# Kernel optimization log

Hardware: AMD Instinct MI355X
Metric: run time of the kernel (lower is better)

Reference implementation:

```python
import jax, jax.numpy as jnp
import numpy as np

DIM = 2048
HEAD_DIM = 128
NHEADS = DIM // HEAD_DIM
ROTARY_BASE = 10000.0
EPS = 1e-6


def rmsnorm(x):
    return x * jax.lax.rsqrt(jnp.mean(x * x, axis=-1, keepdims=True) + EPS)


def make_freqs():
    # (1/base)**linspace(0,1,head_dim//4) concatenated with head_dim//4 zeros
    f = (1.0 / ROTARY_BASE) ** jnp.linspace(0.0, 1.0, HEAD_DIM // 4, dtype=jnp.float32)
    return jnp.concatenate([f, jnp.zeros(HEAD_DIM // 4, dtype=jnp.float32)])  # [head_dim//2]


def rotary(x_NTHD, shift=0):
    T = x_NTHD.shape[1]
    freqs = make_freqs()
    theta = jnp.arange(shift, shift + T, dtype=jnp.float32)[:, None] * freqs[None, :]  # [T, d]
    cos = jnp.cos(theta)[None, :, None, :]
    sin = jnp.sin(theta)[None, :, None, :]
    x1, x2 = jnp.split(x_NTHD, 2, axis=-1)
    y1 = x1 * cos + x2 * sin
    y2 = -x1 * sin + x2 * cos
    return jnp.concatenate([y1, y2], axis=-1)


def setup_inputs() -> dict:
    key = jax.random.key(0)
    ks = jax.random.split(key, 7)
    N, T = 4, 2048
    sd = 1.0 / np.sqrt(DIM)
    x = jax.random.normal(ks[0], (N, T, DIM), dtype=jnp.float32)
    qkv_w = jnp.fmod(jax.random.normal(ks[1], (3, DIM, DIM), dtype=jnp.float32), 2.0) * (sd / 2)
    o_w = jax.random.normal(ks[2], (DIM, DIM), dtype=jnp.float32) * sd
    o_scale = jax.random.normal(ks[3], (DIM,), dtype=jnp.float32) * 0.02
    mlp_w1 = jax.random.normal(ks[4], (4 * DIM, DIM), dtype=jnp.float32) * sd
    mlp_w2 = jax.random.normal(ks[5], (DIM, 4 * DIM), dtype=jnp.float32) * (1.0 / np.sqrt(4 * DIM))
    mlp_scale = jax.random.normal(ks[6], (DIM,), dtype=jnp.float32) * 0.02
    return {"x": x, "qkv_w": qkv_w, "o_w": o_w, "o_scale": o_scale,
            "mlp_w1": mlp_w1, "mlp_w2": mlp_w2, "mlp_scale": mlp_scale}


def reference(x, qkv_w, o_w, o_scale, mlp_w1, mlp_w2, mlp_scale):
    N, T, _ = x.shape
    residual = x
    # RMSNorm -> fused QKV projection
    qkv = rmsnorm(x) @ qkv_w.reshape(3 * DIM, DIM).T            # [N,T,3*dim]
    qkv = qkv.reshape(N, T, 3 * NHEADS, HEAD_DIM)
    q, k, v = jnp.split(qkv, 3, axis=-2)                        # each [N,T,H,hd]
    q, k = rmsnorm(q), rmsnorm(k)                               # QK-norm over head_dim
    q, k = rotary(q), rotary(k)                                 # shift=0 (no kv cache)
    # causal SDPA
    scale = 1.0 / np.sqrt(HEAD_DIM)
    scores = jnp.einsum("bqhd,bkhd->bhqk", q, k) * scale
    mask = jnp.tril(jnp.ones((T, T), dtype=bool))
    scores = jnp.where(mask[None, None], scores, -jnp.inf)
    attn = jax.nn.softmax(scores, axis=-1)
    o = jnp.einsum("bhqk,bkhd->bqhd", attn, v).reshape(N, T, DIM)
    x = residual + (o @ o_w.T) * o_scale
    # MLP: RMSNorm -> up -> relu^2 -> down (scaled)
    h = rmsnorm(x) @ mlp_w1.T
    h = jnp.square(jax.nn.relu(h))
    x = x + (h @ mlp_w2.T) * mlp_scale
    return x, k, v
```

## Files before the change

kernel.cpp:

```cpp
#include <hip/hip_runtime.h>
#include <hip/hip_bf16.h>
#include <cstdint>
#include <cstddef>

typedef unsigned short ushort_t;
typedef __attribute__((ext_vector_type(8))) __bf16 bf16x8;
typedef __attribute__((ext_vector_type(4))) float f32x4;
typedef __attribute__((ext_vector_type(4))) unsigned int u32x4;
typedef __attribute__((ext_vector_type(2))) unsigned int u32x2;

#define LOG2E 1.44269504088896f

__device__ __forceinline__ float bf2f(unsigned short u) {
  union { unsigned int i; float f; } w; w.i = ((unsigned int)u) << 16; return w.f;
}
__device__ __forceinline__ unsigned short f2bf(float f) {
  union { float f; unsigned int i; } w; w.f = f;
  unsigned int u = w.i;
  u += 0x7fffu + ((u >> 16) & 1);
  return (unsigned short)(u >> 16);
}
__device__ __forceinline__ void gld_lds16(const void* g, void* l) {
  __builtin_amdgcn_global_load_lds(
      (const __attribute__((address_space(1))) unsigned int*)g,
      (__attribute__((address_space(3))) unsigned int*)l, 16, 0, 0);
}
__device__ __forceinline__ int swz(int row, int byteoff) {
  return byteoff ^ ((row & 7) << 4);
}

__global__ __launch_bounds__(256)
void cvt_bf16(const float* __restrict__ in, ushort_t* __restrict__ outp, int n) {
  const int i = (blockIdx.x * 256 + threadIdx.x) * 4;
  if (i >= n) return;
  const float4 d = *(const float4*)(in + i);
  u32x2 o;
  o[0] = (unsigned int)f2bf(d.x) | ((unsigned int)f2bf(d.y) << 16);
  o[1] = (unsigned int)f2bf(d.z) | ((unsigned int)f2bf(d.w) << 16);
  *(u32x2*)(outp + i) = o;
}

__device__ __forceinline__ void stage_half(const ushort_t* __restrict__ gsrc,
                                           size_t rstride, ushort_t* ldst, int tid) {
#pragma unroll
  for (int i = 0; i < 2; i++) {
    const int c = i * 512 + tid;
    const int r = c >> 3, col = c & 7;
    gld_lds16(gsrc + (size_t)r * rstride + ((col ^ (r & 7)) << 3), ldst + c * 8);
  }
}

template <int EPI, typename OutT>
__global__ __launch_bounds__(512, 2)
void gemm_bt256(const ushort_t* __restrict__ A, const ushort_t* __restrict__ B,
                OutT* __restrict__ C, const float* __restrict__ Res,
                const float* __restrict__ Scale, int M, int N, int K) {
  __shared__ ushort_t As[2][256 * 64];
  __shared__ ushort_t Bs[2][256 * 64];
  const int tid = threadIdx.x;
  const int wave = tid >> 6, lane = tid & 63;
  const int quad = lane >> 4, l16 = lane & 15;
  const int ntn = N >> 8;
  const int nwg = (M >> 8) * ntn;
  const int lin = blockIdx.y * gridDim.x + blockIdx.x;
  const int wid = (lin & 7) * (nwg >> 3) + (lin >> 3);
  const int bn = (wid % ntn) << 8;
  const int bm = (wid / ntn) << 8;
  const int wm = (wave >> 2) * 128, wn = (wave & 3) * 64;

  f32x4 acc[8][4] = {};

  const ushort_t* aB = A + (size_t)bm * K;
  const ushort_t* bB = B + (size_t)bn * K;
  const int nk = K >> 6;

  stage_half(aB, K, &As[0][0], tid);
  stage_half(aB + (size_t)128 * K, K, &As[0][8192], tid);
  stage_half(bB, K, &Bs[0][0], tid);
  stage_half(bB + (size_t)128 * K, K, &Bs[0][8192], tid);
  asm volatile("s_waitcnt vmcnt(0)" ::: "memory");
  __builtin_amdgcn_sched_barrier(0);
  __builtin_amdgcn_s_barrier();

  for (int t = 0; t < nk; ++t) {
    const int cur = t & 1, nb = cur ^ 1;
    const ushort_t* Ac = &As[cur][0];
    const ushort_t* Bc = &Bs[cur][0];
    const int k0n = (t + 1) << 6;
    const bool pf = (t + 1 < nk);
#pragma unroll
    for (int q = 0; q < 4; q++) {
      const int mh = q >> 1, nh = q & 1;
      bf16x8 af[4][2], bfq[2][2];
#pragma unroll
      for (int j = 0; j < 4; j++) {
        const int row = wm + (mh * 4 + j) * 16 + l16;
#pragma unroll
        for (int ks = 0; ks < 2; ks++)
          af[j][ks] = *(const bf16x8*)&Ac[row * 64 + (swz(row, ks * 64 + quad * 16) >> 1)];
      }
#pragma unroll
      for (int j = 0; j < 2; j++) {
        const int row = wn + (nh * 2 + j) * 16 + l16;
#pragma unroll
        for (int ks = 0; ks < 2; ks++)
          bfq[j][ks] = *(const bf16x8*)&Bc[row * 64 + (swz(row, ks * 64 + quad * 16) >> 1)];
      }
      if (pf) {
        if (q == 0)      stage_half(aB + k0n, K, &As[nb][0], tid);
        else if (q == 1) stage_half(aB + (size_t)128 * K + k0n, K, &As[nb][8192], tid);
        else if (q == 2) {
          stage_half(bB + k0n, K, &Bs[nb][0], tid);
          stage_half(bB + (size_t)128 * K + k0n, K, &Bs[nb][8192], tid);
        }
      }
      __builtin_amdgcn_sched_barrier(0);
      __builtin_amdgcn_s_barrier();
      __builtin_amdgcn_s_setprio(1);
#pragma unroll
      for (int j = 0; j < 4; j++)
#pragma unroll
        for (int n2 = 0; n2 < 2; n2++)
#pragma unroll
          for (int ks = 0; ks < 2; ks++)
            acc[mh * 4 + j][nh * 2 + n2] = __builtin_amdgcn_mfma_f32_16x16x32_bf16(
                af[j][ks], bfq[n2][ks], acc[mh * 4 + j][nh * 2 + n2], 0, 0, 0);
      __builtin_amdgcn_s_setprio(0);
      if (q == 3) {
        asm volatile("s_waitcnt vmcnt(0)" ::: "memory");
      }
      __builtin_amdgcn_sched_barrier(0);
      __builtin_amdgcn_s_barrier();
    }
  }

#pragma unroll
  for (int mt = 0; mt < 8; mt++) {
#pragma unroll
    for (int r = 0; r < 4; r++) {
      const int row = bm + wm + mt * 16 + quad * 4 + r;
      const size_t base = (size_t)row * N;
#pragma unroll
      for (int nt = 0; nt < 4; nt++) {
        const int col = bn + wn + nt * 16 + l16;
        float v = acc[mt][nt][r];
        if (EPI == 1)      v = Res[base + col] + v * Scale[col];
        else if (EPI == 2) { v = fmaxf(v, 0.f); v = v * v; }
        if constexpr (sizeof(OutT) == 2) C[base + col] = f2bf(v);
        else                             C[base + col] = v;
      }
    }
  }
}

__global__ __launch_bounds__(256)
void rmsnorm_k(const float* __restrict__ X, ushort_t* __restrict__ Y) {
  const int row = blockIdx.x, tid = threadIdx.x;
  const float* x = X + (size_t)row * 2048 + tid * 8;
  float v[8];
  *(float4*)&v[0] = *(const float4*)x;
  *(float4*)&v[4] = *(const float4*)(x + 4);
  float ss = 0.f;
#pragma unroll
  for (int i = 0; i < 8; i++) ss += v[i] * v[i];
  for (int o = 32; o; o >>= 1) ss += __shfl_xor(ss, o, 64);
  __shared__ float red[4];
  if ((tid & 63) == 0) red[tid >> 6] = ss;
  __syncthreads();
  const float tot = red[0] + red[1] + red[2] + red[3];
  const float sc = rsqrtf(tot * (1.0f / 2048.0f) + 1e-6f);
  u32x4 o4;
#pragma unroll
  for (int i = 0; i < 4; i++)
    o4[i] = (unsigned int)f2bf(v[2 * i] * sc) | ((unsigned int)f2bf(v[2 * i + 1] * sc) << 16);
  *(u32x4*)(Y + (size_t)row * 2048 + tid * 8) = o4;
}

__global__ __launch_bounds__(256)
void rotary_qk(ushort_t* __restrict__ qkv, float* __restrict__ kout,
               float* __restrict__ vout) {
  const int tid = threadIdx.x, wave = tid >> 6, lane = tid & 63;
  const int unit = blockIdx.x * 4 + wave;
  const int token = unit >> 4, h = unit & 15;
  const int t = token & 2047;
  ushort_t* qrow = qkv + (size_t)token * 6144 + h * 128;
  ushort_t* krow = qrow + 2048;
  const ushort_t* vrow = qrow + 4096;
  float q1 = bf2f(qrow[lane]), q2 = bf2f(qrow[lane + 64]);
  float k1 = bf2f(krow[lane]), k2 = bf2f(krow[lane + 64]);
  float sq = q1 * q1 + q2 * q2, sk = k1 * k1 + k2 * k2;
  for (int o = 32; o; o >>= 1) { sq += __shfl_xor(sq, o, 64); sk += __shfl_xor(sk, o, 64); }
  const float rq = rsqrtf(sq * (1.f / 128.f) + 1e-6f);
  const float rk = rsqrtf(sk * (1.f / 128.f) + 1e-6f);
  q1 *= rq; q2 *= rq; k1 *= rk; k2 *= rk;
  float c = 1.f, s = 0.f;
  if (lane < 32) {
    const float f = exp2f((float)lane * (-13.28771237954945f / 31.0f));
    const float th = (float)t * f;
    s = sinf(th); c = cosf(th);
  }
  const float qy1 = q1 * c + q2 * s, qy2 = -q1 * s + q2 * c;
  const float ky1 = k1 * c + k2 * s, ky2 = -k1 * s + k2 * c;
  const unsigned short qb1 = f2bf(qy1), qb2 = f2bf(qy2);
  const unsigned short kb1 = f2bf(ky1), kb2 = f2bf(ky2);
  qrow[lane] = qb1; qrow[lane + 64] = qb2;
  krow[lane] = kb1; krow[lane + 64] = kb2;
  float* ko = kout + (size_t)token * 2048 + h * 128;
  ko[lane] = bf2f(kb1); ko[lane + 64] = bf2f(kb2);
  float* vo = vout + (size_t)token * 2048 + h * 128;
  vo[lane] = bf2f(vrow[lane]); vo[lane + 64] = bf2f(vrow[lane + 64]);
}

__global__ __launch_bounds__(256)
void transpose_v(const ushort_t* __restrict__ qkv, ushort_t* __restrict__ vt) {
  __shared__ ushort_t tile[128][136];
  const int t16 = blockIdx.x, h = blockIdx.y, b = blockIdx.z;
  const int tid = threadIdx.x;
#pragma unroll
  for (int i = 0; i < 8; i++) {
    const int c = i * 256 + tid;
    const int row = c >> 4, cc = (c & 15) * 8;
    const size_t tok = (size_t)(b * 2048 + t16 * 128 + row);
    u32x4 d = *(const u32x4*)(qkv + tok * 6144 + 4096 + h * 128 + cc);
    *(u32x4*)&tile[row][cc] = d;
  }
  __syncthreads();
#pragma unroll
  for (int i = 0; i < 8; i++) {
    const int c = i * 256 + tid;
    const int hr = c >> 4, tc = (c & 15) * 8;
    u32x4 o;
#pragma unroll
    for (int j = 0; j < 4; j++) {
      const unsigned int lo = tile[tc + 2 * j][hr];
      const unsigned int hi = tile[tc + 2 * j + 1][hr];
      o[j] = lo | (hi << 16);
    }
    *(u32x4*)(vt + ((size_t)(b * 16 + h) * 128 + hr) * 2048 + t16 * 128 + tc) = o;
  }
}

__global__ __launch_bounds__(256)
void attn_k(const ushort_t* __restrict__ qkv, const ushort_t* __restrict__ vt,
            ushort_t* __restrict__ obuf) {
  __shared__ ushort_t kbuf[2][64 * 128];
  __shared__ ushort_t vbuf[2][128 * 64];
  __shared__ ushort_t pbuf[4][32 * 64];
  const int lin = blockIdx.x + (blockIdx.y << 4) + (blockIdx.z << 8);
  const int wid = ((lin & 7) << 7) + (lin >> 3);
  const int qb = 15 - (wid & 15);
  const int h  = (wid >> 4) & 15;
  const int b  = wid >> 8;
  const int tid = threadIdx.x, wave = tid >> 6, lane = tid & 63;
  const int quad = lane >> 4, l16 = lane & 15;
  const float SCALE_L2E = 0.08838834764831845f * 1.44269504088896f;
  const float FML2 = 11.5f * 1.44269504088896f;

  const int nkt = qb * 2 + 2;
  const size_t kb0 = (size_t)(b * 2048) * 6144 + 2048 + h * 128;
  const size_t vt0 = (size_t)(b * 16 + h) * 128 * 2048;

  auto stage = [&](int bu, int kt) {
#pragma unroll
    for (int i = 0; i < 4; i++) {
      const int c = i * 256 + tid;
      const int kr = c >> 4, ck = c & 15;
      gld_lds16(qkv + kb0 + (size_t)(kt * 64 + kr) * 6144 + (ck ^ (kr & 7)) * 8,
                &kbuf[bu][c * 8]);
      const int hr = c >> 3, cv = c & 7;
      gld_lds16(vt + vt0 + (size_t)hr * 2048 + kt * 64 + (cv ^ (hr & 7)) * 8,
                &vbuf[bu][c * 8]);
    }
  };

  bf16x8 qf[2][4];
#pragma unroll
  for (int mt = 0; mt < 2; mt++)
#pragma unroll
    for (int ks = 0; ks < 4; ks++) {
      const int tok = b * 2048 + qb * 128 + wave * 32 + mt * 16 + l16;
      qf[mt][ks] = *(const bf16x8*)(qkv + (size_t)tok * 6144 + h * 128 + ks * 32 + quad * 8);
    }
  f32x4 O[2][8] = {};
  float lrow[2][4] = {};

  stage(0, 0);
  __syncthreads();

  for (int kt = 0; kt < nkt; kt++) {
    const int cur = kt & 1;
    if (kt + 1 < nkt) stage(cur ^ 1, kt + 1);
    __builtin_amdgcn_sched_barrier(0);

    f32x4 S[2][4] = {};
#pragma unroll
    for (int ks = 0; ks < 4; ks++) {
      bf16x8 kf[4];
#pragma unroll
      for (int nt = 0; nt < 4; nt++) {
        const int krow = nt * 16 + l16;
        kf[nt] = *(const bf16x8*)&kbuf[cur][krow * 128 + (swz(krow, ks * 64 + quad * 16) >> 1)];
      }
#pragma unroll
      for (int mt = 0; mt < 2; mt++)
#pragma unroll
        for (int nt = 0; nt < 4; nt++)
          S[mt][nt] = __builtin_amdgcn_mfma_f32_16x16x32_bf16(qf[mt][ks], kf[nt], S[mt][nt], 0, 0, 0);
    }
#pragma unroll
    for (int mt = 0; mt < 2; mt++) {
#pragma unroll
      for (int r = 0; r < 4; r++) {
        const int qr = qb * 128 + wave * 32 + mt * 16 + quad * 4 + r;
        const int prow = mt * 16 + quad * 4 + r;
        float rs = 0.f;
#pragma unroll
        for (int nt = 0; nt < 4; nt++) {
          const int kc = kt * 64 + nt * 16 + l16;
          float p = (kc > qr) ? 0.f : exp2f(fmaf(S[mt][nt][r], SCALE_L2E, -FML2));
          rs += p;
          pbuf[wave][prow * 64 + (swz(prow, (nt * 16 + l16) * 2) >> 1)] = f2bf(p);
        }
        lrow[mt][r] += rs;
      }
    }
#pragma unroll
    for (int ks = 0; ks < 2; ks++) {
      bf16x8 pa[2];
#pragma unroll
      for (int mt = 0; mt < 2; mt++) {
        const int parow = mt * 16 + l16;
        pa[mt] = *(const bf16x8*)&pbuf[wave][parow * 64 + (swz(parow, ks * 64 + quad * 16) >> 1)];
      }
#pragma unroll
      for (int nto = 0; nto < 8; nto++) {
        const int vrow = nto * 16 + l16;
        const bf16x8 vb = *(const bf16x8*)&vbuf[cur][vrow * 64 + (swz(vrow, ks * 64 + quad * 16) >> 1)];
#pragma unroll
        for (int mt = 0; mt < 2; mt++)
          O[mt][nto] = __builtin_amdgcn_mfma_f32_16x16x32_bf16(pa[mt], vb, O[mt][nto], 0, 0, 0);
      }
    }
    __syncthreads();
  }
#pragma unroll
  for (int mt = 0; mt < 2; mt++)
#pragma unroll
    for (int r = 0; r < 4; r++) {
      float ls = lrow[mt][r];
      for (int o = 1; o < 16; o <<= 1) ls += __shfl_xor(ls, o, 64);
      const float inv = 1.0f / ls;
      const int row = b * 2048 + qb * 128 + wave * 32 + mt * 16 + quad * 4 + r;
      const size_t base = (size_t)row * 2048 + h * 128;
#pragma unroll
      for (int nto = 0; nto < 8; nto++)
        obuf[base + nto * 16 + l16] = f2bf(O[mt][nto][r] * inv);
    }
}

extern "C" void kernel_launch(void* const* d_in, const int* in_sizes, int n_in,
                              void* d_out, int out_size, void* d_ws, size_t ws_size,
                              hipStream_t stream) {
  (void)in_sizes; (void)n_in; (void)out_size; (void)ws_size;
  const float* x       = (const float*)d_in[0];
  const float* qkv_w   = (const float*)d_in[1];
  const float* o_w     = (const float*)d_in[2];
  const float* o_scale = (const float*)d_in[3];
  const float* w1      = (const float*)d_in[4];
  const float* w2      = (const float*)d_in[5];
  const float* mscale  = (const float*)d_in[6];
  float* outx = (float*)d_out;
  float* outk = outx + (size_t)16777216;
  float* outv = outk + (size_t)16777216;

  char* ws = (char*)d_ws;
  ushort_t* qkv    = (ushort_t*)(ws + 0);
  ushort_t* vt     = (ushort_t*)(ws + 100663296);
  ushort_t* xn     = (ushort_t*)(ws + 134217728);
  float*    x1     = (float*)   (ws + 167772160);
  ushort_t* qkv_wb = (ushort_t*)(ws + 234881024);
  ushort_t* o_wb   = (ushort_t*)(ws + 260046848);
  ushort_t* w1b    = (ushort_t*)(ws + 268435456);
  ushort_t* w2b    = (ushort_t*)(ws + 301989888);
  ushort_t* hbuf   = (ushort_t*)(ws + 0);

  cvt_bf16<<<12288, 256, 0, stream>>>(qkv_w, qkv_wb, 12582912);
  cvt_bf16<<<4096,  256, 0, stream>>>(o_w,   o_wb,   4194304);
  cvt_bf16<<<16384, 256, 0, stream>>>(w1,    w1b,    16777216);
  cvt_bf16<<<16384, 256, 0, stream>>>(w2,    w2b,    16777216);

  rmsnorm_k<<<8192, 256, 0, stream>>>(x, xn);
  gemm_bt256<0, ushort_t><<<dim3(24, 32), 512, 0, stream>>>(xn, qkv_wb, qkv, nullptr, nullptr, 8192, 6144, 2048);
  rotary_qk<<<32768, 256, 0, stream>>>(qkv, outk, outv);
  transpose_v<<<dim3(16, 16, 4), 256, 0, stream>>>(qkv, vt);
  attn_k<<<dim3(16, 16, 4), 256, 0, stream>>>(qkv, vt, xn );
  gemm_bt256<1, float><<<dim3(8, 32), 512, 0, stream>>>(xn , o_wb, x1, x, o_scale, 8192, 2048, 2048);
  rmsnorm_k<<<8192, 256, 0, stream>>>(x1, xn);
  gemm_bt256<2, ushort_t><<<dim3(32, 32), 512, 0, stream>>>(xn, w1b, hbuf, nullptr, nullptr, 8192, 8192, 2048);
  gemm_bt256<1, float><<<dim3(8, 32), 512, 0, stream>>>(hbuf, w2b, outx, x1, mscale, 8192, 2048, 8192);
}
```

Before: 1.555 ms.

## Restructure GEMM k-loop into two phases reusing B fragments

Replaces the four-quadrant inner schedule with two half-phases per k-step. The B fragments for all four n-tiles are loaded once and reused across both M halves, and the global-to-LDS prefetch is split between the two phases. This cuts the barriers per k-step from eight to three and removes redundant LDS reads of B. The cost is higher register pressure from holding bfr, af and ag at once, which could lower occupancy or cause spills.

```diff
diff --git a/kernel.cpp b/kernel.cpp
--- a/kernel.cpp
+++ b/kernel.cpp
@@ -88,50 +88,64 @@
     const ushort_t* Bc = &Bs[cur][0];
     const int k0n = (t + 1) << 6;
     const bool pf = (t + 1 < nk);
-#pragma unroll
-    for (int q = 0; q < 4; q++) {
-      const int mh = q >> 1, nh = q & 1;
-      bf16x8 af[4][2], bfq[2][2];
-#pragma unroll
-      for (int j = 0; j < 4; j++) {
-        const int row = wm + (mh * 4 + j) * 16 + l16;
+
+    bf16x8 bfr[4][2], af[4][2];
+#pragma unroll
+    for (int n = 0; n < 4; n++) {
+      const int row = wn + n * 16 + l16;
+#pragma unroll
+      for (int ks = 0; ks < 2; ks++)
+        bfr[n][ks] = *(const bf16x8*)&Bc[row * 64 + (swz(row, ks * 64 + quad * 16) >> 1)];
+    }
+#pragma unroll
+    for (int j = 0; j < 4; j++) {
+      const int row = wm + j * 16 + l16;
+#pragma unroll
+      for (int ks = 0; ks < 2; ks++)
+        af[j][ks] = *(const bf16x8*)&Ac[row * 64 + (swz(row, ks * 64 + quad * 16) >> 1)];
+    }
+    if (pf) {
+      stage_half(aB + k0n, K, &As[nb][0], tid);
+      stage_half(aB + (size_t)128 * K + k0n, K, &As[nb][8192], tid);
+    }
+    __builtin_amdgcn_sched_barrier(0);
+    __builtin_amdgcn_s_barrier();
+    __builtin_amdgcn_s_setprio(1);
+#pragma unroll
+    for (int j = 0; j < 4; j++)
+#pragma unroll
+      for (int n = 0; n < 4; n++)
 #pragma unroll
         for (int ks = 0; ks < 2; ks++)
-          af[j][ks] = *(const bf16x8*)&Ac[row * 64 + (swz(row, ks * 64 + quad * 16) >> 1)];
-      }
-#pragma unroll
-      for (int j = 0; j < 2; j++) {
-        const int row = wn + (nh * 2 + j) * 16 + l16;
+          acc[j][n] = __builtin_amdgcn_mfma_f32_16x16x32_bf16(af[j][ks], bfr[n][ks], acc[j][n], 0, 0, 0);
+    __builtin_amdgcn_s_setprio(0);
+
+    bf16x8 ag[4][2];
+#pragma unroll
+    for (int j = 0; j < 4; j++) {
+      const int row = wm + 64 + j * 16 + l16;
+#pragma unroll
+      for (int ks = 0; ks < 2; ks++)
+        ag[j][ks] = *(const bf16x8*)&Ac[row * 64 + (swz(row, ks * 64 + quad * 16) >> 1)];
+    }
+    if (pf) {
+      stage_half(bB + k0n, K, &Bs[nb][0], tid);
+      stage_half(bB + (size_t)128 * K + k0n, K, &Bs[nb][8192], tid);
+    }
+    __builtin_amdgcn_sched_barrier(0);
+    __builtin_amdgcn_s_barrier();
+    __builtin_amdgcn_s_setprio(1);
+#pragma unroll
+    for (int j = 0; j < 4; j++)
+#pragma unroll
+      for (int n = 0; n < 4; n++)
 #pragma unroll
         for (int ks = 0; ks < 2; ks++)
-          bfq[j][ks] = *(const bf16x8*)&Bc[row * 64 + (swz(row, ks * 64 + quad * 16) >> 1)];
-      }
-      if (pf) {
-        if (q == 0)      stage_half(aB + k0n, K, &As[nb][0], tid);
-        else if (q == 1) stage_half(aB + (size_t)128 * K + k0n, K, &As[nb][8192], tid);
-        else if (q == 2) {
-          stage_half(bB + k0n, K, &Bs[nb][0], tid);
-          stage_half(bB + (size_t)128 * K + k0n, K, &Bs[nb][8192], tid);
-        }
-      }
-      __builtin_amdgcn_sched_barrier(0);
-      __builtin_amdgcn_s_barrier();
-      __builtin_amdgcn_s_setprio(1);
-#pragma unroll
-      for (int j = 0; j < 4; j++)
-#pragma unroll
-        for (int n2 = 0; n2 < 2; n2++)
-#pragma unroll
-          for (int ks = 0; ks < 2; ks++)
-            acc[mh * 4 + j][nh * 2 + n2] = __builtin_amdgcn_mfma_f32_16x16x32_bf16(
-                af[j][ks], bfq[n2][ks], acc[mh * 4 + j][nh * 2 + n2], 0, 0, 0);
-      __builtin_amdgcn_s_setprio(0);
-      if (q == 3) {
-        asm volatile("s_waitcnt vmcnt(0)" ::: "memory");
-      }
-      __builtin_amdgcn_sched_barrier(0);
-      __builtin_amdgcn_s_barrier();
-    }
+          acc[4 + j][n] = __builtin_amdgcn_mfma_f32_16x16x32_bf16(ag[j][ks], bfr[n][ks], acc[4 + j][n], 0, 0, 0);
+    __builtin_amdgcn_s_setprio(0);
+    asm volatile("s_waitcnt vmcnt(0)" ::: "memory");
+    __builtin_amdgcn_sched_barrier(0);
+    __builtin_amdgcn_s_barrier();
   }
 
 #pragma unroll
```

New measurement: 1.429 ms. -8.1%, faster.

## Switch GEMM to 4-stage BK=32 LDS pipeline with one barrier per step

Applied to the files above, without the earlier changes.

Replaces the double-buffered BK=64 GEMM main loop, which had four sub-phases and two barriers per phase, with a four-buffer BK=32 ring. Loads for tile t+3 are issued at the top of each iteration and completion is tracked with graded vmcnt waits, so only one barrier is needed per k-step. The goal is deeper prefetch and less synchronisation overhead. It drops the XOR swizzle on the LDS layout, which risks LDS bank conflicts on the fragment reads, and it halves the MFMA work per barrier.

```diff
diff --git a/kernel.cpp b/kernel.cpp
--- a/kernel.cpp
+++ b/kernel.cpp
@@ -40,23 +40,13 @@
   *(u32x2*)(outp + i) = o;
 }
 
-__device__ __forceinline__ void stage_half(const ushort_t* __restrict__ gsrc,
-                                           size_t rstride, ushort_t* ldst, int tid) {
-#pragma unroll
-  for (int i = 0; i < 2; i++) {
-    const int c = i * 512 + tid;
-    const int r = c >> 3, col = c & 7;
-    gld_lds16(gsrc + (size_t)r * rstride + ((col ^ (r & 7)) << 3), ldst + c * 8);
-  }
-}
-
 template <int EPI, typename OutT>
 __global__ __launch_bounds__(512, 2)
 void gemm_bt256(const ushort_t* __restrict__ A, const ushort_t* __restrict__ B,
                 OutT* __restrict__ C, const float* __restrict__ Res,
                 const float* __restrict__ Scale, int M, int N, int K) {
-  __shared__ ushort_t As[2][256 * 64];
-  __shared__ ushort_t Bs[2][256 * 64];
+  __shared__ ushort_t As[4][256 * 32];
+  __shared__ ushort_t Bs[4][256 * 32];
   const int tid = threadIdx.x;
   const int wave = tid >> 6, lane = tid & 63;
   const int quad = lane >> 4, l16 = lane & 15;
@@ -72,66 +62,52 @@
 
   const ushort_t* aB = A + (size_t)bm * K;
   const ushort_t* bB = B + (size_t)bn * K;
-  const int nk = K >> 6;
-
-  stage_half(aB, K, &As[0][0], tid);
-  stage_half(aB + (size_t)128 * K, K, &As[0][8192], tid);
-  stage_half(bB, K, &Bs[0][0], tid);
-  stage_half(bB + (size_t)128 * K, K, &Bs[0][8192], tid);
-  asm volatile("s_waitcnt vmcnt(0)" ::: "memory");
+  const int nk = K >> 5;
+
+  const int r0 = tid >> 2, c0 = (tid & 3) * 8;
+  const ushort_t* a0 = aB + (size_t)r0 * K + c0;
+  const ushort_t* a1 = a0 + (size_t)128 * K;
+  const ushort_t* b0 = bB + (size_t)r0 * K + c0;
+  const ushort_t* b1 = b0 + (size_t)128 * K;
+
+  auto stage = [&](int tt) {
+    ushort_t* da = &As[tt & 3][0];
+    ushort_t* db = &Bs[tt & 3][0];
+    const int ko = tt << 5;
+    gld_lds16(a0 + ko, da + tid * 8);
+    gld_lds16(a1 + ko, da + 4096 + tid * 8);
+    gld_lds16(b0 + ko, db + tid * 8);
+    gld_lds16(b1 + ko, db + 4096 + tid * 8);
+  };
+
+  stage(0); stage(1); stage(2);
+  asm volatile("s_waitcnt vmcnt(8)" ::: "memory");
   __builtin_amdgcn_sched_barrier(0);
   __builtin_amdgcn_s_barrier();
 
   for (int t = 0; t < nk; ++t) {
-    const int cur = t & 1, nb = cur ^ 1;
-    const ushort_t* Ac = &As[cur][0];
-    const ushort_t* Bc = &Bs[cur][0];
-    const int k0n = (t + 1) << 6;
-    const bool pf = (t + 1 < nk);
-#pragma unroll
-    for (int q = 0; q < 4; q++) {
-      const int mh = q >> 1, nh = q & 1;
-      bf16x8 af[4][2], bfq[2][2];
-#pragma unroll
-      for (int j = 0; j < 4; j++) {
-        const int row = wm + (mh * 4 + j) * 16 + l16;
-#pragma unroll
-        for (int ks = 0; ks < 2; ks++)
-          af[j][ks] = *(const bf16x8*)&Ac[row * 64 + (swz(row, ks * 64 + quad * 16) >> 1)];
-      }
-#pragma unroll
-      for (int j = 0; j < 2; j++) {
-        const int row = wn + (nh * 2 + j) * 16 + l16;
-#pragma unroll
-        for (int ks = 0; ks < 2; ks++)
-          bfq[j][ks] = *(const bf16x8*)&Bc[row * 64 + (swz(row, ks * 64 + quad * 16) >> 1)];
-      }
-      if (pf) {
-        if (q == 0)      stage_half(aB + k0n, K, &As[nb][0], tid);
-        else if (q == 1) stage_half(aB + (size_t)128 * K + k0n, K, &As[nb][8192], tid);
-        else if (q == 2) {
-          stage_half(bB + k0n, K, &Bs[nb][0], tid);
-          stage_half(bB + (size_t)128 * K + k0n, K, &Bs[nb][8192], tid);
-        }
-      }
-      __builtin_amdgcn_sched_barrier(0);
-      __builtin_amdgcn_s_barrier();
-      __builtin_amdgcn_s_setprio(1);
-#pragma unroll
-      for (int j = 0; j < 4; j++)
-#pragma unroll
-        for (int n2 = 0; n2 < 2; n2++)
-#pragma unroll
-          for (int ks = 0; ks < 2; ks++)
-            acc[mh * 4 + j][nh * 2 + n2] = __builtin_amdgcn_mfma_f32_16x16x32_bf16(
-                af[j][ks], bfq[n2][ks], acc[mh * 4 + j][nh * 2 + n2], 0, 0, 0);
-      __builtin_amdgcn_s_setprio(0);
-      if (q == 3) {
-        asm volatile("s_waitcnt vmcnt(0)" ::: "memory");
-      }
-      __builtin_amdgcn_sched_barrier(0);
-      __builtin_amdgcn_s_barrier();
-    }
+    if (t + 3 < nk) stage(t + 3);
+    const ushort_t* Ac = &As[t & 3][0];
+    const ushort_t* Bc = &Bs[t & 3][0];
+    bf16x8 af[8], bfr[4];
+#pragma unroll
+    for (int mt = 0; mt < 8; mt++)
+      af[mt] = *(const bf16x8*)&Ac[(wm + mt * 16 + l16) * 32 + quad * 8];
+#pragma unroll
+    for (int n = 0; n < 4; n++)
+      bfr[n] = *(const bf16x8*)&Bc[(wn + n * 16 + l16) * 32 + quad * 8];
+    __builtin_amdgcn_s_setprio(1);
+#pragma unroll
+    for (int mt = 0; mt < 8; mt++)
+#pragma unroll
+      for (int n = 0; n < 4; n++)
+        acc[mt][n] = __builtin_amdgcn_mfma_f32_16x16x32_bf16(af[mt], bfr[n], acc[mt][n], 0, 0, 0);
+    __builtin_amdgcn_s_setprio(0);
+    if (t + 3 < nk)      { asm volatile("s_waitcnt vmcnt(8)" ::: "memory"); }
+    else if (t + 2 < nk) { asm volatile("s_waitcnt vmcnt(4)" ::: "memory"); }
+    else if (t + 1 < nk) { asm volatile("s_waitcnt vmcnt(0)" ::: "memory"); }
+    __builtin_amdgcn_sched_barrier(0);
+    __builtin_amdgcn_s_barrier();
   }
 
 #pragma unroll
```

Measured after the change: 1.775 ms. +14.1%, slower.
